# Kernel optimization log

Measured on AMD Instinct MI355X. Metric: run time of the kernel, lower is better.

The kernel has to match this reference:

```python
import jax, jax.numpy as jnp
import numpy as np

S = 3
K = 3
K2 = K * K
BN_EPS = 1e-5


def _conv(x, w, pad=0):
    return jax.lax.conv_general_dilated(
        x, w, window_strides=(1, 1), padding=[(pad, pad), (pad, pad)],
        dimension_numbers=('NCHW', 'OIHW', 'NCHW'))


def _adaptive_avg_pool(x, s):
    # PyTorch adaptive_avg_pool2d semantics: bin i covers [floor(i*H/s), ceil((i+1)*H/s))
    B, C, H, W = x.shape
    rows = []
    for i in range(s):
        h0, h1 = (i * H) // s, -(-((i + 1) * H) // s)
        cols = []
        for j in range(s):
            w0, w1 = (j * W) // s, -(-((j + 1) * W) // s)
            cols.append(x[:, :, h0:h1, w0:w1].mean(axis=(2, 3)))
        rows.append(jnp.stack(cols, axis=-1))
    return jnp.stack(rows, axis=-2)  # (B, C, s, s)


def _forward(c4, c5, w_to_fuse, bn_gamma, bn_beta, w_c4_proc, w_conv1,
             w_reshape, w_proj, w_sim4, w_sim5, kg_w1, kg_b1, kg_w2, kg_b2,
             mask_raw):
    B, C4, H, W = c4.shape
    H2, W2 = c5.shape[2], c5.shape[3]
    # nearest upsample c5 -> (H, W)
    ih = (jnp.arange(H) * H2) // H
    iw = (jnp.arange(W) * W2) // W
    c5_up = c5[:, :, ih][:, :, :, iw]

    c4_proc = _conv(c4, w_c4_proc, pad=1)
    c5_proc = _conv(c5_up, w_conv1)  # adaptive pool to (H,W) is identity here
    fused = c4_proc + c5_proc

    # to_fuse 1x1 conv -> BatchNorm (training-mode batch stats) -> SiLU
    y = _conv(fused, w_to_fuse)
    mu = y.mean(axis=(0, 2, 3), keepdims=True)
    var = y.var(axis=(0, 2, 3), keepdims=True)
    y = (y - mu) / jnp.sqrt(var + BN_EPS)
    X = jax.nn.silu(y * bn_gamma[None, :, None, None] + bn_beta[None, :, None, None])

    # patch descriptors and similarity (dot)
    p4 = _conv(_adaptive_avg_pool(c4, S), w_sim4)    # (B, sim, S, S)
    p5 = _conv(_adaptive_avg_pool(c5_up, S), w_sim5)
    sim = (p4 * p5).sum(axis=1)                      # (B, S, S)

    gated = sim.reshape(B, S * S) * jax.nn.sigmoid(mask_raw)[None, :]  # (B, S2)
    k_in = gated.reshape(B * S * S, 1)
    h = jax.nn.relu(k_in @ kg_w1.T + kg_b1)
    kernels = jax.nn.softmax((h @ kg_w2.T + kg_b2).reshape(B, S * S, K2), axis=-1)

    # unfold X: (B, C, K2, H, W) with torch row-major kernel-position order
    pad = K // 2
    Xp = jnp.pad(X, ((0, 0), (0, 0), (pad, pad), (pad, pad)))
    patches = jnp.stack([Xp[:, :, dy:dy + H, dx:dx + W]
                         for dy in range(K) for dx in range(K)], axis=2)

    # per-pixel patch index -> per-pixel kernel
    y_idx = jnp.clip((jnp.arange(H) * S) // H, 0, S - 1)
    x_idx = jnp.clip((jnp.arange(W) * S) // W, 0, S - 1)
    pidx = y_idx[:, None] * S + x_idx[None, :]       # (H, W) int
    kmap = kernels[:, pidx, :]                       # (B, H, W, K2)

    out = jnp.einsum('bckhw,bhwk->bchw', patches, kmap)

    fused_red = _conv(_conv(fused, w_reshape), w_proj)
    return out + fused_red


def setup_inputs() -> dict:
    key = jax.random.key(0)
    ks = jax.random.split(key, 16)
    B, C4, C5, H, W = 8, 256, 512, 64, 64
    OC, SIM, FR, HID = 256, 64, 128, 16
    n = jax.random.normal
    return {
        'c4': n(ks[0], (B, C4, H, W), dtype=jnp.float32),
        'c5': n(ks[1], (B, C5, H // 2, W // 2), dtype=jnp.float32),
        'w_to_fuse': n(ks[2], (OC, C4, 1, 1), dtype=jnp.float32) * 0.05,
        'bn_gamma': jnp.ones((OC,), dtype=jnp.float32),
        'bn_beta': jnp.zeros((OC,), dtype=jnp.float32),
        'w_c4_proc': n(ks[3], (C4, C4, 3, 3), dtype=jnp.float32) * 0.05,
        'w_conv1': n(ks[4], (C4, C5, 1, 1), dtype=jnp.float32) * 0.05,
        'w_reshape': n(ks[5], (FR, C4, 1, 1), dtype=jnp.float32) * 0.05,
        'w_proj': n(ks[6], (OC, FR, 1, 1), dtype=jnp.float32) * 0.05,
        'w_sim4': n(ks[7], (SIM, C4, 1, 1), dtype=jnp.float32) * 0.05,
        'w_sim5': n(ks[8], (SIM, C5, 1, 1), dtype=jnp.float32) * 0.05,
        'kg_w1': n(ks[9], (HID, 1), dtype=jnp.float32) * 0.5,
        'kg_b1': n(ks[10], (HID,), dtype=jnp.float32) * 0.1,
        'kg_w2': n(ks[11], (K2, HID), dtype=jnp.float32) * 0.5,
        'kg_b2': n(ks[12], (K2,), dtype=jnp.float32) * 0.1,
        'mask_raw': jnp.zeros((K2,), dtype=jnp.float32),
    }


def reference(c4, c5, w_to_fuse, bn_gamma, bn_beta, w_c4_proc, w_conv1,
              w_reshape, w_proj, w_sim4, w_sim5, kg_w1, kg_b1, kg_w2, kg_b2,
              mask_raw):
    return _forward(c4, c5, w_to_fuse, bn_gamma, bn_beta, w_c4_proc, w_conv1,
                    w_reshape, w_proj, w_sim4, w_sim5, kg_w1, kg_b1, kg_w2,
                    kg_b2, mask_raw)
```

## Files before the change

kernel.cpp:

```cpp
#include <hip/hip_runtime.h>
#include <cstddef>

#define B_   8
#define C4_  256
#define C5_  512
#define OC_  256
#define FR_  128
#define H_   64
#define W_   64
#define HW_  4096

typedef unsigned short u16;
typedef __bf16 bf16x8 __attribute__((ext_vector_type(8)));
typedef float floatx16 __attribute__((ext_vector_type(16)));

__device__ __forceinline__ u16 f2b(float x) {
    unsigned int u = __float_as_uint(x);
    return (u16)((u + 0x7FFFu + ((u >> 16) & 1u)) >> 16);
}
__device__ __forceinline__ float b2f(u16 x) {
    return __uint_as_float(((unsigned int)x) << 16);
}

__device__ __forceinline__ void gll16(const u16* g, char* l) {
    __builtin_amdgcn_global_load_lds(
        (const __attribute__((address_space(1))) void*)g,
        (__attribute__((address_space(3))) void*)l, 16, 0, 0);
}

__global__ __launch_bounds__(256) void pack_all(
    const float* __restrict__ w3, const float* __restrict__ w1,
    const float* __restrict__ wtf,
    const float* __restrict__ wp, const float* __restrict__ wr,
    const float* __restrict__ in4, const float* __restrict__ in5,
    u16* __restrict__ A3f, u16* __restrict__ A1f, u16* __restrict__ Wtff,
    u16* __restrict__ Wefff, u16* __restrict__ c4t, u16* __restrict__ c5f)
{
    __shared__ float sT[16448];
    const int t = threadIdx.x;
    const int blk = blockIdx.x;

    if (blk < 3072) {
        int i = blk * 256 + t;
        if (i < 589824) {
            int j  = i & 7;
            int l  = (i >> 3) & 63;
            int ks = (i >> 9) & 15;
            int ot = (i >> 13) & 7;
            int tap = i >> 16;
            int oc = ot * 32 + (l & 31);
            int c  = ks * 16 + ((l >> 5) << 3) + j;
            A3f[i] = f2b(w3[((size_t)oc * 256 + c) * 9 + tap]);
        } else if (i < 720896) {
            int i2 = i - 589824;
            int j  = i2 & 7;
            int l  = (i2 >> 3) & 63;
            int ks = (i2 >> 9) & 31;
            int ot = i2 >> 14;
            int oc = ot * 32 + (l & 31);
            int c  = ks * 16 + ((l >> 5) << 3) + j;
            A1f[i2] = f2b(w1[(size_t)oc * 512 + c]);
        } else {
            int i3 = i - 720896;
            int j  = i3 & 7;
            int l  = (i3 >> 3) & 63;
            int ks = (i3 >> 9) & 15;
            int ot = i3 >> 13;
            int oc = ot * 32 + (l & 31);
            int c  = ks * 16 + ((l >> 5) << 3) + j;
            Wtff[i3] = f2b(wtf[(size_t)oc * 256 + c]);
        }
    } else if (blk < 3328) {
        const int oc = blk - 3072, c = t;
        float s = 0.f;
        for (int f = 0; f < 128; ++f)
            s += wp[oc * 128 + f] * wr[f * 256 + c];
        int ot = oc >> 5;
        int lf = (oc & 31) + (((c >> 3) & 1) << 5);
        int ks = c >> 4;
        int j  = c & 7;
        Wefff[(((size_t)ot * 16 + ks) * 64 + lf) * 8 + j] = f2b(s);
    } else {
        const int id = blk - 3328;
        const int b = id / 96, x = id % 96;
        if (x < 64) {
            const int h = x;
            const int w = t & 63, cg = t >> 6;
            for (int i = 0; i < 64; ++i) {
                int c = cg * 64 + i;
                sT[w * 257 + c] = in4[(((size_t)b * 256 + c) * 64 + h) * 64 + w];
            }
            __syncthreads();
            for (int i = 0; i < 16; ++i) {
                int ww = cg * 16 + i;
                int c0 = (t & 63) * 4;
                ushort4 v;
                v.x = f2b(sT[ww * 257 + c0]);
                v.y = f2b(sT[ww * 257 + c0 + 1]);
                v.z = f2b(sT[ww * 257 + c0 + 2]);
                v.w = f2b(sT[ww * 257 + c0 + 3]);
                *(ushort4*)&c4t[(((size_t)b * 66 + h + 1) * 72 + ww + 1) * 256 + c0] = v;
            }
        } else {
            const int h2 = x - 64;
            const int w = t & 31, cg = t >> 5;
            for (int i = 0; i < 64; ++i) {
                int c = cg * 64 + i;
                sT[w * 513 + c] = in5[(((size_t)b * 512 + c) * 32 + h2) * 32 + w];
            }
            __syncthreads();
            u16* dstb = c5f + (size_t)(b * 32 + h2) * 32768;
            for (int i = 0; i < 32; ++i) {
                int id2 = i * 256 + t;
                int j0 = (id2 & 1) * 4;
                int l  = (id2 >> 1) & 63;
                int ks = (id2 >> 7) & 31;
                int n  = (id2 >> 12) & 1;
                int ch = ks * 16 + ((l >> 5) << 3) + j0;
                int w2 = (n * 32 + (l & 31)) >> 1;
                ushort4 v;
                v.x = f2b(sT[w2 * 513 + ch]);
                v.y = f2b(sT[w2 * 513 + ch + 1]);
                v.z = f2b(sT[w2 * 513 + ch + 2]);
                v.w = f2b(sT[w2 * 513 + ch + 3]);
                *(ushort4*)&dstb[id2 * 4] = v;
            }
        }
    }
}

__global__ __launch_bounds__(512, 1) void fuse_all(
    const u16* __restrict__ c4t, const u16* __restrict__ c5f,
    const u16* __restrict__ A3f, const u16* __restrict__ A1f,
    const u16* __restrict__ Wtff, const u16* __restrict__ Wefff,
    u16* __restrict__ yb, u16* __restrict__ outb, float* __restrict__ sums)
{
    extern __shared__ char smem[];
    float* lsum = (float*)(smem + 65536);
    float* lsq  = lsum + 256;

    const int t   = threadIdx.x;
    const int lin = blockIdx.x;
    const int d   = ((lin & 7) << 5) + (lin >> 3);
    const int b   = d >> 5;
    const int rp  = d & 31;
    const int h0  = rp * 2;

    const int l   = t & 63;
    const int w8  = t >> 6;
    const int og  = w8 >> 1;
    const int pg  = w8 & 1;
    const int lc  = l & 31;
    const int lg  = l >> 5;

    const int ocb = og * 64;
    const int otb = og * 2;
    const int gseg = (l & 7) ^ (l >> 3);

    if (t < 256) { lsum[t] = 0.f; lsq[t] = 0.f; }

    floatx16 acc[2][2];
    #pragma unroll
    for (int m = 0; m < 2; ++m)
        #pragma unroll
        for (int n = 0; n < 2; ++n)
            #pragma unroll
            for (int r = 0; r < 16; ++r)
                acc[m][n][r] = 0.f;

    bf16x8 areg[9][2];
    #pragma unroll
    for (int tap = 0; tap < 9; ++tap)
        #pragma unroll
        for (int m = 0; m < 2; ++m)
            areg[tap][m] = *(const bf16x8*)(A3f + ((((size_t)tap * 8 + otb + m) * 16 + 0) * 64 + l) * 8);

    for (int c0 = 0; c0 < 256; c0 += 64) {
        __syncthreads();
        for (int q = w8; q < 36; q += 8) {
            const int r  = q / 9;
            const int cq = (q - r * 9) * 8;
            const u16* gp = c4t + ((((size_t)b * 66 + h0 + r) * 72 + cq + (l >> 3)) << 8)
                          + c0 + gseg * 8;
            gll16(gp, smem + (r * 72 + cq) * 128);
        }
        __syncthreads();

        const int ksb = c0 >> 4;
        #pragma unroll
        for (int kst = 0; kst < 4; ++kst) {
            const int ksgN = (kst < 3) ? (ksb + kst + 1)
                                       : ((c0 < 192) ? ksb + 4 : 0);
            #pragma unroll
            for (int ky = 0; ky < 3; ++ky) {
                #pragma unroll
                for (int kx = 0; kx < 3; ++kx) {
                    const int tap = ky * 3 + kx;
                    bf16x8 bb[2];
                    #pragma unroll
                    for (int n = 0; n < 2; ++n) {
                        const int pix = (pg + ky) * 72 + n * 32 + lc + kx;
                        const int seg = (kst * 2 + lg) ^ (pix & 7);
                        bb[n] = *(const bf16x8*)(smem + pix * 128 + (seg << 4));
                    }
                    #pragma unroll
                    for (int m = 0; m < 2; ++m)
                        #pragma unroll
                        for (int n = 0; n < 2; ++n)
                            acc[m][n] = __builtin_amdgcn_mfma_f32_32x32x16_bf16(
                                areg[tap][m], bb[n], acc[m][n], 0, 0, 0);
                    #pragma unroll
                    for (int m = 0; m < 2; ++m)
                        areg[tap][m] = *(const bf16x8*)(A3f + ((((size_t)tap * 8 + otb + m) * 16 + ksgN) * 64 + l) * 8);
                }
            }
        }
    }

    const u16* c5b = c5f + (size_t)(b * 32 + rp) * 32768;
    {
        bf16x8 a1[2][2], b1[2][2];
        #pragma unroll
        for (int m = 0; m < 2; ++m) {
            a1[0][m] = *(const bf16x8*)(A1f + ((((size_t)otb + m) * 32 + 0) * 64 + l) * 8);
            b1[0][m] = *(const bf16x8*)(c5b + (((size_t)m * 32 + 0) * 64 + l) * 8);
        }
        #pragma unroll
        for (int ks = 0; ks < 32; ++ks) {
            const int cur = ks & 1, nxt = cur ^ 1;
            if (ks < 31) {
                #pragma unroll
                for (int m = 0; m < 2; ++m) {
                    a1[nxt][m] = *(const bf16x8*)(A1f + ((((size_t)otb + m) * 32 + ks + 1) * 64 + l) * 8);
                    b1[nxt][m] = *(const bf16x8*)(c5b + (((size_t)m * 32 + ks + 1) * 64 + l) * 8);
                }
            }
            #pragma unroll
            for (int m = 0; m < 2; ++m)
                #pragma unroll
                for (int n = 0; n < 2; ++n)
                    acc[m][n] = __builtin_amdgcn_mfma_f32_32x32x16_bf16(
                        a1[cur][m], b1[cur][n], acc[m][n], 0, 0, 0);
        }
    }

    __syncthreads();
    #pragma unroll
    for (int n = 0; n < 2; ++n) {
        const int px = pg * 64 + n * 32 + lc;
        #pragma unroll
        for (int m = 0; m < 2; ++m) {
            #pragma unroll
            for (int rq = 0; rq < 4; ++rq) {
                const int oc = ocb + m * 32 + rq * 8 + lg * 4;
                const int slot = oc >> 3;
                ushort4 v;
                v.x = f2b(acc[m][n][rq * 4 + 0]);
                v.y = f2b(acc[m][n][rq * 4 + 1]);
                v.z = f2b(acc[m][n][rq * 4 + 2]);
                v.w = f2b(acc[m][n][rq * 4 + 3]);
                *(ushort4*)(smem + px * 512 + ((slot ^ (px & 31)) << 4) + (oc & 7) * 2) = v;
            }
        }
    }
    __syncthreads();

    const bool isY = (w8 < 4);
    const u16* Wf  = isY ? Wtff : Wefff;
    u16* dst       = isY ? yb : outb;
    const int ot2  = (w8 & 3) * 2;

    #pragma unroll
    for (int ph = 0; ph < 2; ++ph) {
        floatx16 a2[2][2];
        #pragma unroll
        for (int m = 0; m < 2; ++m)
            #pragma unroll
            for (int n = 0; n < 2; ++n)
                #pragma unroll
                for (int r = 0; r < 16; ++r)
                    a2[m][n][r] = 0.f;

        bf16x8 wreg[2][2];
        #pragma unroll
        for (int m = 0; m < 2; ++m)
            wreg[0][m] = *(const bf16x8*)(Wf + ((((size_t)ot2 + m) * 16 + 0) * 64 + l) * 8);

        #pragma unroll
        for (int ks = 0; ks < 16; ++ks) {
            const int cur = ks & 1, nxt = cur ^ 1;
            if (ks < 15) {
                #pragma unroll
                for (int m = 0; m < 2; ++m)
                    wreg[nxt][m] = *(const bf16x8*)(Wf + ((((size_t)ot2 + m) * 16 + ks + 1) * 64 + l) * 8);
            }
            bf16x8 bb[2];
            #pragma unroll
            for (int n = 0; n < 2; ++n) {
                const int px = ph * 64 + n * 32 + lc;
                const int slot = ks * 2 + lg;
                bb[n] = *(const bf16x8*)(smem + px * 512 + ((slot ^ (px & 31)) << 4));
            }
            #pragma unroll
            for (int m = 0; m < 2; ++m)
                #pragma unroll
                for (int n = 0; n < 2; ++n)
                    a2[m][n] = __builtin_amdgcn_mfma_f32_32x32x16_bf16(
                        wreg[cur][m], bb[n], a2[m][n], 0, 0, 0);
        }

        #pragma unroll
        for (int n = 0; n < 2; ++n) {
            const int px = ph * 64 + n * 32 + lc;
            const int row = px >> 6, wcol = px & 63;
            const size_t gp = (((size_t)b * 64 + h0 + row) * 64 + wcol) * 256;
            #pragma unroll
            for (int m = 0; m < 2; ++m) {
                #pragma unroll
                for (int rq = 0; rq < 4; ++rq) {
                    const int ocl = (w8 & 3) * 64 + m * 32 + rq * 8 + lg * 4;
                    ushort4 v;
                    v.x = f2b(a2[m][n][rq * 4 + 0]);
                    v.y = f2b(a2[m][n][rq * 4 + 1]);
                    v.z = f2b(a2[m][n][rq * 4 + 2]);
                    v.w = f2b(a2[m][n][rq * 4 + 3]);
                    *(ushort4*)&dst[gp + ocl] = v;
                }
            }
        }

        if (isY) {
            #pragma unroll
            for (int m = 0; m < 2; ++m) {
                #pragma unroll
                for (int r = 0; r < 16; ++r) {
                    float s = 0.f, q = 0.f;
                    #pragma unroll
                    for (int n = 0; n < 2; ++n) {
                        float v = a2[m][n][r];
                        s += v; q += v * v;
                    }
                    #pragma unroll
                    for (int off = 1; off < 32; off <<= 1) {
                        s += __shfl_xor(s, off);
                        q += __shfl_xor(q, off);
                    }
                    if (lc == 0) {
                        const int ocl = (w8 & 3) * 64 + m * 32 + (r & 3) + 8 * (r >> 2) + 4 * lg;
                        atomicAdd(&lsum[ocl], s);
                        atomicAdd(&lsq[ocl], q);
                    }
                }
            }
        }
    }

    __syncthreads();
    if (t < 256) {
        atomicAdd(&sums[t], lsum[t]);
        atomicAdd(&sums[256 + t], lsq[t]);
    }
}

__global__ __launch_bounds__(256) void pool_both(const float* __restrict__ in4,
                                                 const float* __restrict__ in5,
                                                 float* __restrict__ pool4,
                                                 float* __restrict__ pool5)
{
    __shared__ float colsum[4][64];
    const int i = blockIdx.x, b = blockIdx.z;
    const int t = threadIdx.x;
    const int ch = t >> 6, w = t & 63;
    const int h0 = (i * 64) / 3, h1 = ((i + 1) * 64 + 2) / 3;
    const bool is4 = (blockIdx.y < 64);
    const int cg = is4 ? blockIdx.y : (blockIdx.y - 64);
    const int c = cg * 4 + ch;

    float s = 0.f;
    for (int h = h0; h < h1; ++h) {
        float v = is4 ? in4[(((size_t)b * 256 + c) * 64 + h) * 64 + w]
                      : in5[(((size_t)b * 512 + c) * 32 + (h >> 1)) * 32 + (w >> 1)];
        s += v;
    }
    colsum[ch][w] = s;
    __syncthreads();
    if (t < 12) {
        int c2 = t / 3, j = t % 3;
        int w0 = (j * 64) / 3, w1 = ((j + 1) * 64 + 2) / 3;
        float tot = 0.f;
        for (int x = w0; x < w1; ++x) tot += colsum[c2][x];
        float r = tot / (float)((h1 - h0) * (w1 - w0));
        if (is4) pool4[(((size_t)b * 256 + cg * 4 + c2) * 3 + i) * 3 + j] = r;
        else     pool5[(((size_t)b * 512 + cg * 4 + c2) * 3 + i) * 3 + j] = r;
    }
}

__global__ __launch_bounds__(64) void sim_mlp(
    const float* __restrict__ pool4, const float* __restrict__ pool5,
    const float* __restrict__ w4, const float* __restrict__ w5,
    const float* __restrict__ kgw1, const float* __restrict__ kgb1,
    const float* __restrict__ kgw2, const float* __restrict__ kgb2,
    const float* __restrict__ mask, float* __restrict__ kers)
{
    const int r = blockIdx.x, b = blockIdx.y, m = threadIdx.x;
    float p4 = 0.f, p5 = 0.f;
    for (int c = 0; c < C4_; ++c)
        p4 += w4[(size_t)m * C4_ + c] * pool4[((size_t)b * C4_ + c) * 9 + r];
    for (int c = 0; c < C5_; ++c)
        p5 += w5[(size_t)m * C5_ + c] * pool5[((size_t)b * C5_ + c) * 9 + r];
    float v = p4 * p5;
    #pragma unroll
    for (int off = 32; off; off >>= 1) v += __shfl_down(v, off);
    if (m == 0) {
        float g = v * (1.f / (1.f + __expf(-mask[r])));
        float hb[16];
        #pragma unroll
        for (int j = 0; j < 16; ++j) hb[j] = fmaxf(g * kgw1[j] + kgb1[j], 0.f);
        float lg[9], mx = -1e30f;
        #pragma unroll
        for (int k = 0; k < 9; ++k) {
            float s = kgb2[k];
            #pragma unroll
            for (int j = 0; j < 16; ++j) s += kgw2[k * 16 + j] * hb[j];
            lg[k] = s;
            mx = fmaxf(mx, s);
        }
        float den = 0.f;
        #pragma unroll
        for (int k = 0; k < 9; ++k) { lg[k] = __expf(lg[k] - mx); den += lg[k]; }
        float inv = 1.f / den;
        #pragma unroll
        for (int k = 0; k < 9; ++k)
            kers[((size_t)b * 9 + r) * 9 + k] = lg[k] * inv;
    }
}

__global__ __launch_bounds__(256) void dynconv_bn(const u16* __restrict__ yb,
                                                  const u16* __restrict__ outb,
                                                  const float* __restrict__ sums,
                                                  const float* __restrict__ gamma,
                                                  const float* __restrict__ beta,
                                                  const float* __restrict__ kers,
                                                  float* __restrict__ out)
{
    __shared__ float sX[4][10][66];
    __shared__ float sK[81];
    __shared__ float sAB[8];
    const int t = threadIdx.x;
    const int r0 = blockIdx.x * 8, cg = blockIdx.y, b = blockIdx.z;
    const int ch = t >> 6, w = t & 63;
    const int c = cg * 4 + ch;

    if (t < 4) {
        const int cc = cg * 4 + t;
        const float n = (float)(B_ * HW_);
        float mu  = sums[cc] / n;
        float var = sums[256 + cc] / n - mu * mu;
        float a = gamma[cc] * rsqrtf(var + 1e-5f);
        sAB[t]     = a;
        sAB[4 + t] = beta[cc] - mu * a;
    }
    if (t < 81) sK[t] = kers[(size_t)b * 81 + t];
    __syncthreads();

    for (int idx = t; idx < 660; idx += 256) {
        int rr = idx / 66, cl = idx % 66;
        int gh = r0 - 1 + rr, gw = cl - 1;
        float v0 = 0.f, v1 = 0.f, v2 = 0.f, v3 = 0.f;
        if (gh >= 0 && gh < H_ && gw >= 0 && gw < W_) {
            ushort4 u = *(const ushort4*)&yb[((((size_t)b * 64 + gh) * 64 + gw) << 8) + cg * 4];
            float z;
            z = fmaf(sAB[0], b2f(u.x), sAB[4]); v0 = z / (1.f + __expf(-z));
            z = fmaf(sAB[1], b2f(u.y), sAB[5]); v1 = z / (1.f + __expf(-z));
            z = fmaf(sAB[2], b2f(u.z), sAB[6]); v2 = z / (1.f + __expf(-z));
            z = fmaf(sAB[3], b2f(u.w), sAB[7]); v3 = z / (1.f + __expf(-z));
        }
        sX[0][rr][cl] = v0;
        sX[1][rr][cl] = v1;
        sX[2][rr][cl] = v2;
        sX[3][rr][cl] = v3;
    }
    __syncthreads();

    const int rx = (w * 3) >> 6;
    for (int hh = 0; hh < 8; ++hh) {
        int h = r0 + hh;
        int ry = (h * 3) >> 6;
        const float* kp = &sK[(ry * 3 + rx) * 9];
        float acc = 0.f;
        #pragma unroll
        for (int dy = 0; dy < 3; ++dy)
            #pragma unroll
            for (int dx = 0; dx < 3; ++dx)
                acc += kp[dy * 3 + dx] * sX[ch][hh + dy][w + dx];
        acc += b2f(outb[((((size_t)b * 64 + h) * 64 + w) << 8) + c]);
        out[(((size_t)b * 256 + c) * H_ + h) * W_ + w] = acc;
    }
}

extern "C" void kernel_launch(void* const* d_in, const int* in_sizes, int n_in,
                              void* d_out, int out_size, void* d_ws, size_t ws_size,
                              hipStream_t stream)
{
    const float* c4       = (const float*)d_in[0];
    const float* c5       = (const float*)d_in[1];
    const float* w_to_fuse= (const float*)d_in[2];
    const float* bn_gamma = (const float*)d_in[3];
    const float* bn_beta  = (const float*)d_in[4];
    const float* w_c4_proc= (const float*)d_in[5];
    const float* w_conv1  = (const float*)d_in[6];
    const float* w_reshape= (const float*)d_in[7];
    const float* w_proj   = (const float*)d_in[8];
    const float* w_sim4   = (const float*)d_in[9];
    const float* w_sim5   = (const float*)d_in[10];
    const float* kg_w1    = (const float*)d_in[11];
    const float* kg_b1    = (const float*)d_in[12];
    const float* kg_w2    = (const float*)d_in[13];
    const float* kg_b2    = (const float*)d_in[14];
    const float* mask_raw = (const float*)d_in[15];

    float* out = (float*)d_out;

    u16*   yb    = (u16*)d_ws;
    u16*   outb  = yb + 8388608;
    u16*   c4t   = outb + 8388608;
    u16*   c5f   = c4t + 9732096;
    u16*   A3f   = c5f + 8388608;
    u16*   A1f   = A3f + 589824;
    u16*   Wtff  = A1f + 131072;
    u16*   Wefff = Wtff + 65536;
    float* pool4 = (float*)(Wefff + 65536);
    float* pool5 = pool4 + 18432;
    float* sums  = pool5 + 36864;
    float* kers  = sums + 512;

    hipMemsetAsync(sums, 0, 512 * sizeof(float), stream);
    hipMemsetAsync(c4t, 0, (size_t)9732096 * sizeof(u16), stream);

    pack_all<<<4096, 256, 0, stream>>>(w_c4_proc, w_conv1, w_to_fuse,
                                       w_proj, w_reshape, c4, c5,
                                       A3f, A1f, Wtff, Wefff, c4t, c5f);

    fuse_all<<<256, 512, 67584, stream>>>(c4t, c5f, A3f, A1f, Wtff, Wefff,
                                          yb, outb, sums);

    pool_both<<<dim3(3, 192, 8), 256, 0, stream>>>(c4, c5, pool4, pool5);

    sim_mlp<<<dim3(9, 8), 64, 0, stream>>>(pool4, pool5, w_sim4, w_sim5,
                                           kg_w1, kg_b1, kg_w2, kg_b2,
                                           mask_raw, kers);

    dynconv_bn<<<dim3(8, 64, 8), 256, 0, stream>>>(yb, outb, sums,
                                                   bn_gamma, bn_beta, kers, out);
}
```

Measured before the change: 228.1 us.

## Fuse adaptive pooling into pack kernel and remap dynconv block order

Drops the separate pool_both kernel. The pack kernel now computes the 3x3 adaptive-pool partial sums from the transposed tiles already held in shared memory and accumulates them into pool4/pool5 with atomics. The bin-area normalisation moves into sim_mlp as a squared scale on the similarity, which is valid because each of the pool4 and pool5 means carries the same bin area and the product is linear. dynconv_bn now uses a 1D grid with a swizzled block index, likely to improve locality across batches or XCDs. The exchange is extra atomic traffic and shared-memory reads in the pack kernel, and float atomics make the summation order non-deterministic.

```diff
diff --git a/kernel.cpp b/kernel.cpp
--- a/kernel.cpp
+++ b/kernel.cpp
@@ -34,7 +34,8 @@
     const float* __restrict__ wp, const float* __restrict__ wr,
     const float* __restrict__ in4, const float* __restrict__ in5,
     u16* __restrict__ A3f, u16* __restrict__ A1f, u16* __restrict__ Wtff,
-    u16* __restrict__ Wefff, u16* __restrict__ c4t, u16* __restrict__ c5f)
+    u16* __restrict__ Wefff, u16* __restrict__ c4t, u16* __restrict__ c5f,
+    float* __restrict__ pool4, float* __restrict__ pool5)
 {
     __shared__ float sT[16448];
     const int t = threadIdx.x;
@@ -101,6 +102,26 @@
                 v.w = f2b(sT[ww * 257 + c0 + 3]);
                 *(ushort4*)&c4t[(((size_t)b * 66 + h + 1) * 72 + ww + 1) * 256 + c0] = v;
             }
+            {
+                const int c = t;
+                float cs[3];
+                #pragma unroll
+                for (int j = 0; j < 3; ++j) {
+                    const int w0 = (j * 64) / 3, w1 = ((j + 1) * 64 + 2) / 3;
+                    float s = 0.f;
+                    for (int w2 = w0; w2 < w1; ++w2) s += sT[w2 * 257 + c];
+                    cs[j] = s;
+                }
+                #pragma unroll
+                for (int i = 0; i < 3; ++i) {
+                    const int h0 = (i * 64) / 3, h1 = ((i + 1) * 64 + 2) / 3;
+                    if (h >= h0 && h < h1) {
+                        #pragma unroll
+                        for (int j = 0; j < 3; ++j)
+                            atomicAdd(&pool4[((size_t)b * 256 + c) * 9 + i * 3 + j], cs[j]);
+                    }
+                }
+            }
         } else {
             const int h2 = x - 64;
             const int w = t & 31, cg = t >> 5;
@@ -124,6 +145,30 @@
                 v.z = f2b(sT[w2 * 513 + ch + 2]);
                 v.w = f2b(sT[w2 * 513 + ch + 3]);
                 *(ushort4*)&dstb[id2 * 4] = v;
+            }
+            #pragma unroll
+            for (int half = 0; half < 2; ++half) {
+                const int cc = half * 256 + t;
+                float cs[3];
+                #pragma unroll
+                for (int j = 0; j < 3; ++j) {
+                    const int w0 = (j * 64) / 3, w1 = ((j + 1) * 64 + 2) / 3;
+                    float s = 0.f;
+                    for (int w2 = w0; w2 < w1; ++w2) s += sT[(w2 >> 1) * 513 + cc];
+                    cs[j] = s;
+                }
+                #pragma unroll
+                for (int i = 0; i < 3; ++i) {
+                    const int h0 = (i * 64) / 3, h1 = ((i + 1) * 64 + 2) / 3;
+                    const int wt = (int)(2 * h2 >= h0 && 2 * h2 < h1)
+                                 + (int)(2 * h2 + 1 >= h0 && 2 * h2 + 1 < h1);
+                    if (wt) {
+                        const float fw = (float)wt;
+                        #pragma unroll
+                        for (int j = 0; j < 3; ++j)
+                            atomicAdd(&pool5[((size_t)b * 512 + cc) * 9 + i * 3 + j], fw * cs[j]);
+                    }
+                }
             }
         }
     }
@@ -362,39 +407,6 @@
     }
 }
 
-__global__ __launch_bounds__(256) void pool_both(const float* __restrict__ in4,
-                                                 const float* __restrict__ in5,
-                                                 float* __restrict__ pool4,
-                                                 float* __restrict__ pool5)
-{
-    __shared__ float colsum[4][64];
-    const int i = blockIdx.x, b = blockIdx.z;
-    const int t = threadIdx.x;
-    const int ch = t >> 6, w = t & 63;
-    const int h0 = (i * 64) / 3, h1 = ((i + 1) * 64 + 2) / 3;
-    const bool is4 = (blockIdx.y < 64);
-    const int cg = is4 ? blockIdx.y : (blockIdx.y - 64);
-    const int c = cg * 4 + ch;
-
-    float s = 0.f;
-    for (int h = h0; h < h1; ++h) {
-        float v = is4 ? in4[(((size_t)b * 256 + c) * 64 + h) * 64 + w]
-                      : in5[(((size_t)b * 512 + c) * 32 + (h >> 1)) * 32 + (w >> 1)];
-        s += v;
-    }
-    colsum[ch][w] = s;
-    __syncthreads();
-    if (t < 12) {
-        int c2 = t / 3, j = t % 3;
-        int w0 = (j * 64) / 3, w1 = ((j + 1) * 64 + 2) / 3;
-        float tot = 0.f;
-        for (int x = w0; x < w1; ++x) tot += colsum[c2][x];
-        float r = tot / (float)((h1 - h0) * (w1 - w0));
-        if (is4) pool4[(((size_t)b * 256 + cg * 4 + c2) * 3 + i) * 3 + j] = r;
-        else     pool5[(((size_t)b * 512 + cg * 4 + c2) * 3 + i) * 3 + j] = r;
-    }
-}
-
 __global__ __launch_bounds__(64) void sim_mlp(
     const float* __restrict__ pool4, const float* __restrict__ pool5,
     const float* __restrict__ w4, const float* __restrict__ w5,
@@ -412,6 +424,11 @@
     #pragma unroll
     for (int off = 32; off; off >>= 1) v += __shfl_down(v, off);
     if (m == 0) {
+        const int ri = r / 3, rj = r % 3;
+        const int h0 = (ri * 64) / 3, h1 = ((ri + 1) * 64 + 2) / 3;
+        const int w0 = (rj * 64) / 3, w1 = ((rj + 1) * 64 + 2) / 3;
+        const float inv = 1.f / (float)((h1 - h0) * (w1 - w0));
+        v *= inv * inv;
         float g = v * (1.f / (1.f + __expf(-mask[r])));
         float hb[16];
         #pragma unroll
@@ -428,10 +445,10 @@
         float den = 0.f;
         #pragma unroll
         for (int k = 0; k < 9; ++k) { lg[k] = __expf(lg[k] - mx); den += lg[k]; }
-        float inv = 1.f / den;
+        float inv2 = 1.f / den;
         #pragma unroll
         for (int k = 0; k < 9; ++k)
-            kers[((size_t)b * 9 + r) * 9 + k] = lg[k] * inv;
+            kers[((size_t)b * 9 + r) * 9 + k] = lg[k] * inv2;
     }
 }
 
@@ -447,7 +464,11 @@
     __shared__ float sK[81];
     __shared__ float sAB[8];
     const int t = threadIdx.x;
-    const int r0 = blockIdx.x * 8, cg = blockIdx.y, b = blockIdx.z;
+    const int lin = blockIdx.x;
+    const int dd  = ((lin & 7) << 9) | (lin >> 3);
+    const int b   = dd >> 9;
+    const int r0  = ((dd >> 6) & 7) * 8;
+    const int cg  = dd & 63;
     const int ch = t >> 6, w = t & 63;
     const int c = cg * 4 + ch;
 
@@ -534,22 +555,21 @@
     float* sums  = pool5 + 36864;
     float* kers  = sums + 512;
 
-    hipMemsetAsync(sums, 0, 512 * sizeof(float), stream);
+    hipMemsetAsync(pool4, 0, (size_t)(18432 + 36864 + 512) * sizeof(float), stream);
     hipMemsetAsync(c4t, 0, (size_t)9732096 * sizeof(u16), stream);
 
     pack_all<<<4096, 256, 0, stream>>>(w_c4_proc, w_conv1, w_to_fuse,
                                        w_proj, w_reshape, c4, c5,
-                                       A3f, A1f, Wtff, Wefff, c4t, c5f);
+                                       A3f, A1f, Wtff, Wefff, c4t, c5f,
+                                       pool4, pool5);
 
     fuse_all<<<256, 512, 67584, stream>>>(c4t, c5f, A3f, A1f, Wtff, Wefff,
                                           yb, outb, sums);
-
-    pool_both<<<dim3(3, 192, 8), 256, 0, stream>>>(c4, c5, pool4, pool5);
 
     sim_mlp<<<dim3(9, 8), 64, 0, stream>>>(pool4, pool5, w_sim4, w_sim5,
                                            kg_w1, kg_b1, kg_w2, kg_b2,
                                            mask_raw, kers);
 
-    dynconv_bn<<<dim3(8, 64, 8), 256, 0, stream>>>(yb, outb, sums,
-                                                   bn_gamma, bn_beta, kers, out);
-}
+    dynconv_bn<<<4096, 256, 0, stream>>>(yb, outb, sums,
+                                         bn_gamma, bn_beta, kers, out);
+}
```

Result: faster. 220.6 us (-3.3%).
